# Kernel optimization log

Measured on AMD Instinct MI355X. Metric: run time of the kernel, lower is better.

The kernel has to match this reference:

```python
import jax, jax.numpy as jnp
import numpy as np

K = 7      # unfold_size
P = 3      # unfold_size // 2
EPS = 1e-5 # batchnorm eps


def _conv1x1(x, w, b=None):
    # x: (B,C,H,W), w: (O,C)
    y = jnp.einsum('bchw,oc->bohw', x, w)
    if b is not None:
        y = y + b[None, :, None, None]
    return y


def _bn(x, g, b, m, v):
    # eval-mode batchnorm over channel axis 1
    inv = jax.lax.rsqrt(v + EPS)
    return (x - m[None, :, None, None]) * (g * inv)[None, :, None, None] + b[None, :, None, None]


def setup_inputs() -> dict:
    key = jax.random.key(0)
    ks = jax.random.split(key, 18)
    B, C, MID, H, W = 8, 256, 64, 64, 64
    rn = lambda k, s, sc=1.0: jax.random.normal(k, s, dtype=jnp.float32) * sc
    ru = lambda k, s: jax.random.uniform(k, s, dtype=jnp.float32)
    return {
        'x':     rn(ks[0], (B, C, H, W)),
        'w_red': rn(ks[1], (MID, C), 0.05),
        'w_c':   rn(ks[2], (3, MID, MID, 3, 3), 0.05),
        'b_c':   rn(ks[3], (3, MID), 0.05),
        'bn_g':  ru(ks[4], (3, MID)) * 0.5 + 0.75,
        'bn_b':  rn(ks[5], (3, MID), 0.05),
        'bn_m':  rn(ks[6], (3, MID), 0.05),
        'bn_v':  ru(ks[7], (3, MID)) + 0.5,
        'w_out': rn(ks[8], (C, MID), 0.05),
        'b_out': rn(ks[9], (C,), 0.05),
        'bno_g': ru(ks[10], (C,)) * 0.5 + 0.75,
        'bno_b': rn(ks[11], (C,), 0.05),
        'bno_m': rn(ks[12], (C,), 0.05),
        'bno_v': ru(ks[13], (C,)) + 0.5,
        'w_f1':  rn(ks[14], (C, C), 0.05),
        'b_f1':  rn(ks[15], (C,), 0.05),
        'w_f2':  rn(ks[16], (C, C), 0.05),
        'b_f2':  rn(ks[17], (C,), 0.05),
    }


def reference(x, w_red, w_c, b_c, bn_g, bn_b, bn_m, bn_v,
              w_out, b_out, bno_g, bno_b, bno_m, bno_v,
              w_f1, b_f1, w_f2, b_f2):
    B, C, H, W = x.shape
    MID = w_red.shape[0]

    # channel reduction + L2 normalize over channels (F.normalize, eps=1e-12)
    q = _conv1x1(x, w_red)                                   # (B,MID,H,W)
    q = q / jnp.maximum(jnp.linalg.norm(q, axis=1, keepdims=True), 1e-12)

    # SelfCorrelationComputation: unfold KxK with padding P, multiply by center, clamp >= 0
    qp = jnp.pad(q, ((0, 0), (0, 0), (P, P), (P, P)))
    pats = jnp.stack([qp[:, :, i:i + H, j:j + W]
                      for i in range(K) for j in range(K)], axis=2)  # (B,MID,K*K,H,W)
    ss = jnp.maximum(pats * q[:, :, None], 0.0)              # (B,MID,49,H,W)

    # SelfSimilarityEncoder: conv3d with (1,ksize,ksize) kernel == batched 2D conv over (u,v)
    ss = ss.transpose(0, 3, 4, 1, 2).reshape(B * H * W, MID, K, K)  # (B*HW,MID,K,K)
    dn = ('NCHW', 'OIHW', 'NCHW')
    y = ss
    for i in range(3):  # unfold_size // 2 blocks; 7 -> 5 -> 3 -> 1
        y = jax.lax.conv_general_dilated(y, w_c[i], (1, 1), 'VALID', dimension_numbers=dn)
        y = y + b_c[i][None, :, None, None]
        y = jnp.maximum(_bn(y, bn_g[i], bn_b[i], bn_m[i], bn_v[i]), 0.0)
    y = y.mean(axis=(-1, -2)).reshape(B, H, W, MID).transpose(0, 3, 1, 2)  # (B,MID,H,W)
    feat = _bn(_conv1x1(y, w_out, b_out), bno_g, bno_b, bno_m, bno_v)      # (B,C,H,W)

    # residual + FFN (1x1 conv -> relu -> 1x1 conv)
    out = x + feat
    out = _conv1x1(jnp.maximum(_conv1x1(out, w_f1, b_f1), 0.0), w_f2, b_f2)
    return out
```

## Files before the change

### kernel.cpp

```cpp
#include <hip/hip_runtime.h>
#include <stdint.h>


typedef __attribute__((ext_vector_type(8))) __bf16 bf16x8;
typedef __attribute__((ext_vector_type(4))) float f32x4;

__device__ __forceinline__ ushort f2bf(float f) {
  __bf16 h = (__bf16)f;
  return __builtin_bit_cast(ushort, h);
}
__device__ __forceinline__ float bfu(ushort h) {
  return __builtin_bit_cast(float, ((uint32_t)h) << 16);
}
__device__ __forceinline__ f32x4 mfma16(bf16x8 a, bf16x8 b, f32x4 c) {
  return __builtin_amdgcn_mfma_f32_16x16x32_bf16(a, b, c, 0, 0, 0);
}

union BV8 { uint4 v; ushort u[8]; };

#define OFF_WRT 0u
#define OFF_WCB 65536u
#define OFF_SHC 286720u
#define OFF_WOB 287488u
#define OFF_SHO 320256u
#define OFF_WF1 321280u
#define OFF_WF2 452352u
#define OFF_QN  583424u
#define OFF_Y   4777728u

__global__ __launch_bounds__(256) void k_prep(
    const float* __restrict__ w_red, const float* __restrict__ w_c, const float* __restrict__ b_c,
    const float* __restrict__ bn_g, const float* __restrict__ bn_b, const float* __restrict__ bn_m,
    const float* __restrict__ bn_v, const float* __restrict__ w_out, const float* __restrict__ b_out,
    const float* __restrict__ bno_g, const float* __restrict__ bno_b, const float* __restrict__ bno_m,
    const float* __restrict__ bno_v, const float* __restrict__ w_f1, const float* __restrict__ w_f2,
    float* __restrict__ w_red_t, ushort* __restrict__ wc_b, float* __restrict__ shift_c,
    ushort* __restrict__ w_out_b, float* __restrict__ shift_o,
    ushort* __restrict__ w_f1_b, ushort* __restrict__ w_f2_b)
{
  int i = blockIdx.x * 256 + threadIdx.x;
  if (i < 16384) {
    int c = i >> 6, m = i & 63;
    w_red_t[i] = w_red[m * 256 + c];
    return;
  }
  i -= 16384;
  if (i < 110592) {
    int c = i & 63, o = (i >> 6) & 63, st = i >> 12;
    int tap = st % 9, s = st / 9;
    float sc = bn_g[s * 64 + o] * rsqrtf(bn_v[s * 64 + o] + 1e-5f);
    wc_b[i] = f2bf(w_c[((s * 64 + o) * 64 + c) * 9 + tap] * sc);
    return;
  }
  i -= 110592;
  if (i < 192) {
    int s = i >> 6, o = i & 63;
    float sc = bn_g[s * 64 + o] * rsqrtf(bn_v[s * 64 + o] + 1e-5f);
    shift_c[i] = (b_c[i] - bn_m[i]) * sc + bn_b[i];
    return;
  }
  i -= 192;
  if (i < 16384) {
    int o = i >> 6;
    float sc = bno_g[o] * rsqrtf(bno_v[o] + 1e-5f);
    w_out_b[i] = f2bf(w_out[i] * sc);
    return;
  }
  i -= 16384;
  if (i < 256) {
    float sc = bno_g[i] * rsqrtf(bno_v[i] + 1e-5f);
    shift_o[i] = (b_out[i] - bno_m[i]) * sc + bno_b[i];
    return;
  }
  i -= 256;
  if (i < 65536) { w_f1_b[i] = f2bf(w_f1[i]); return; }
  i -= 65536;
  if (i < 65536) { w_f2_b[i] = f2bf(w_f2[i]); return; }
}

__global__ __launch_bounds__(256) void k_qnorm(
    const float* __restrict__ x, const float* __restrict__ w_red_t, ushort* __restrict__ qn)
{
  __shared__ float xs[64 * 64];
  __shared__ float wls[64 * 64];
  __shared__ float part[64 * 16];
  __shared__ float sinv[64];

  const int tid = threadIdx.x;
  const int pix0 = blockIdx.x * 64;
  const int b = pix0 >> 12;
  const int hw0 = pix0 & 4095;
  const int pxq = tid & 15, mq = tid >> 4;
  const int lr = tid >> 2, lseg = tid & 3;

  float acc[4][4] = {};

  for (int c0 = 0; c0 < 256; c0 += 64) {
    const float4* xg = (const float4*)(x + (size_t)(b * 256 + c0 + lr) * 4096 + hw0 + lseg * 16);
    float4* xd = (float4*)(xs + lr * 64 + lseg * 16);
    const float4* wg = (const float4*)(w_red_t + (c0 + lr) * 64 + lseg * 16);
    float4* wd = (float4*)(wls + lr * 64 + lseg * 16);
#pragma unroll
    for (int j = 0; j < 4; ++j) xd[j] = xg[j];
#pragma unroll
    for (int j = 0; j < 4; ++j) wd[j] = wg[j];
    __syncthreads();
    for (int c = 0; c < 64; ++c) {
      float4 xv = *(const float4*)(xs + c * 64 + pxq * 4);
      float4 wv = *(const float4*)(wls + c * 64 + mq * 4);
      float xa[4] = {xv.x, xv.y, xv.z, xv.w};
      float wa[4] = {wv.x, wv.y, wv.z, wv.w};
#pragma unroll
      for (int mi = 0; mi < 4; ++mi)
#pragma unroll
        for (int pi = 0; pi < 4; ++pi)
          acc[mi][pi] = fmaf(wa[mi], xa[pi], acc[mi][pi]);
    }
    __syncthreads();
  }

#pragma unroll
  for (int pi = 0; pi < 4; ++pi) {
    float s = 0.f;
#pragma unroll
    for (int mi = 0; mi < 4; ++mi) s += acc[mi][pi] * acc[mi][pi];
    part[(pxq * 4 + pi) * 16 + mq] = s;
  }
  __syncthreads();
  if (tid < 64) {
    float s = 0.f;
#pragma unroll
    for (int k = 0; k < 16; ++k) s += part[tid * 16 + k];
    sinv[tid] = 1.0f / fmaxf(sqrtf(s), 1e-12f);
  }
  __syncthreads();
#pragma unroll
  for (int pi = 0; pi < 4; ++pi) {
    const int px = pxq * 4 + pi;
    const float inv = sinv[px];
    ushort4 v;
    v.x = f2bf(acc[0][pi] * inv);
    v.y = f2bf(acc[1][pi] * inv);
    v.z = f2bf(acc[2][pi] * inv);
    v.w = f2bf(acc[3][pi] * inv);
    *(ushort4*)(qn + (size_t)(pix0 + px) * 64 + mq * 4) = v;
  }
}

#define ENC_RING 7168
#define ENC_O1   14336
#define SMEM_ENC 79872

__device__ __forceinline__ void store_act(ushort* buf, int pos, int n, int q, int o0,
                                          f32x4 acc, float4 sh) {
  ushort4 v;
  v.x = f2bf(fmaxf(acc[0] + sh.x, 0.0f));
  v.y = f2bf(fmaxf(acc[1] + sh.y, 0.0f));
  v.z = f2bf(fmaxf(acc[2] + sh.z, 0.0f));
  v.w = f2bf(fmaxf(acc[3] + sh.w, 0.0f));
  const int chunk = (o0 >> 3) + (q >> 1);
  *(ushort4*)(buf + (pos * 16 + n) * 64 + ((chunk ^ (n & 7)) * 8) + (q & 1) * 4) = v;
}

__device__ __forceinline__ void build_row(
    ushort* dstslot, const ushort* __restrict__ qn,
    int b, int tr, int tc, int ir, int tid)
{
  for (int u0 = tid; u0 < 896; u0 += 256) {
    const int ch = u0 & 7, px = (u0 >> 3) & 15, dv = u0 >> 7;
    const int ph = tr + (px >> 2), pw = tc + (px & 3);
    const int nh = ph + ir - 3, nw = pw + dv - 3;
    uint4 ov4;
    if ((unsigned)nh < 64u && (unsigned)nw < 64u) {
      BV8 cv; cv.v = *(const uint4*)(qn + (size_t)((b << 12) + ph * 64 + pw) * 64 + ch * 8);
      BV8 nv; nv.v = *(const uint4*)(qn + (size_t)((b << 12) + nh * 64 + nw) * 64 + ch * 8);
      BV8 ov;
#pragma unroll
      for (int j = 0; j < 8; ++j)
        ov.u[j] = f2bf(fmaxf(bfu(nv.u[j]) * bfu(cv.u[j]), 0.0f));
      ov4 = ov.v;
    } else {
      ov4 = make_uint4(0u, 0u, 0u, 0u);
    }
    *(uint4*)(dstslot + (dv * 16 + px) * 64 + ((ch ^ (px & 7)) * 8)) = ov4;
  }
}

__global__ __launch_bounds__(256, 2) void k_encoder(
    const ushort* __restrict__ qn, const ushort* __restrict__ wc_b,
    const float* __restrict__ shift_c, ushort* __restrict__ yout)
{
  extern __shared__ char smem[];
  ushort* enc = (ushort*)smem;
  ushort* o1 = enc + ENC_O1;

  const int tid = threadIdx.x;
  const int b = blockIdx.z;
  const int tr = blockIdx.y * 4;
  const int tc = blockIdx.x * 4;

  const int lane = tid & 63, wv = tid >> 6;
  const int n = lane & 15, q = lane >> 4;
  const int o0 = wv * 16;
  const int sw = n & 7;
  const int rowoff = n * 64;
  const int c0 = ((0 + q) ^ sw) * 8;
  const int c1 = ((4 + q) ^ sw) * 8;

  bf16x8 af[18];
#pragma unroll
  for (int t = 0; t < 9; ++t) {
    af[t * 2]     = *(const bf16x8*)(wc_b + (t * 64 + o0 + n) * 64 + q * 8);
    af[t * 2 + 1] = *(const bf16x8*)(wc_b + (t * 64 + o0 + n) * 64 + 32 + q * 8);
  }

  const f32x4 zero = {0.f, 0.f, 0.f, 0.f};
  f32x4 acc[5][5];
#pragma unroll
  for (int u = 0; u < 5; ++u)
#pragma unroll
    for (int v = 0; v < 5; ++v) acc[u][v] = zero;

  build_row(enc, qn, b, tr, tc, 0, tid);
  __syncthreads();

#pragma unroll
  for (int ir = 0; ir < 7; ++ir) {
    if (ir < 6)
      build_row(enc + ((ir + 1) & 1) * ENC_RING, qn, b, tr, tc, ir + 1, tid);
    {
      const ushort* rowb = enc + (ir & 1) * ENC_RING + rowoff;
      bf16x8 rf0[7], rf1[7];
#pragma unroll
      for (int j = 0; j < 7; ++j) {
        rf0[j] = *(const bf16x8*)(rowb + j * 1024 + c0);
        rf1[j] = *(const bf16x8*)(rowb + j * 1024 + c1);
      }
#pragma unroll
      for (int u = 0; u < 5; ++u) {
        const int du = ir - u;
        if (du >= 0 && du < 3) {
#pragma unroll
          for (int dv = 0; dv < 3; ++dv)
#pragma unroll
            for (int v = 0; v < 5; ++v) {
              acc[u][v] = mfma16(af[(du * 3 + dv) * 2],     rf0[v + dv], acc[u][v]);
              acc[u][v] = mfma16(af[(du * 3 + dv) * 2 + 1], rf1[v + dv], acc[u][v]);
            }
        }
      }
    }
    if (ir < 6) __syncthreads();
  }

  {
    const float4 sh = *(const float4*)(shift_c + o0 + q * 4);
#pragma unroll
    for (int u = 0; u < 5; ++u)
#pragma unroll
      for (int v = 0; v < 5; ++v)
        store_act(o1, u * 5 + v, n, q, o0, acc[u][v], sh);
  }
  __syncthreads();

  {
#pragma unroll
    for (int t = 0; t < 9; ++t) {
      af[t * 2]     = *(const bf16x8*)(wc_b + 9 * 4096 + (t * 64 + o0 + n) * 64 + q * 8);
      af[t * 2 + 1] = *(const bf16x8*)(wc_b + 9 * 4096 + (t * 64 + o0 + n) * 64 + 32 + q * 8);
    }
    f32x4 acc2[3][3];
#pragma unroll
    for (int u = 0; u < 3; ++u)
#pragma unroll
      for (int v = 0; v < 3; ++v) acc2[u][v] = zero;

#pragma unroll
    for (int ir = 0; ir < 5; ++ir) {
      const ushort* rowb = o1 + ir * 5 * 1024 + rowoff;
      bf16x8 rf0[5], rf1[5];
#pragma unroll
      for (int j = 0; j < 5; ++j) {
        rf0[j] = *(const bf16x8*)(rowb + j * 1024 + c0);
        rf1[j] = *(const bf16x8*)(rowb + j * 1024 + c1);
      }
#pragma unroll
      for (int u = 0; u < 3; ++u) {
        const int du = ir - u;
        if (du >= 0 && du < 3) {
#pragma unroll
          for (int dv = 0; dv < 3; ++dv)
#pragma unroll
            for (int v = 0; v < 3; ++v) {
              acc2[u][v] = mfma16(af[(du * 3 + dv) * 2],     rf0[v + dv], acc2[u][v]);
              acc2[u][v] = mfma16(af[(du * 3 + dv) * 2 + 1], rf1[v + dv], acc2[u][v]);
            }
        }
      }
    }
    const float4 sh = *(const float4*)(shift_c + 64 + o0 + q * 4);
#pragma unroll
    for (int u = 0; u < 3; ++u)
#pragma unroll
      for (int v = 0; v < 3; ++v)
        store_act(enc, u * 3 + v, n, q, o0, acc2[u][v], sh);
  }
  __syncthreads();

  {
#pragma unroll
    for (int t = 0; t < 9; ++t) {
      af[t * 2]     = *(const bf16x8*)(wc_b + 18 * 4096 + (t * 64 + o0 + n) * 64 + q * 8);
      af[t * 2 + 1] = *(const bf16x8*)(wc_b + 18 * 4096 + (t * 64 + o0 + n) * 64 + 32 + q * 8);
    }
    f32x4 a0 = zero, a1 = zero;
#pragma unroll
    for (int tap = 0; tap < 9; ++tap) {
      const ushort* rA = enc + tap * 1024 + rowoff;
      a0 = mfma16(af[tap * 2],     *(const bf16x8*)(rA + c0), a0);
      a1 = mfma16(af[tap * 2 + 1], *(const bf16x8*)(rA + c1), a1);
    }
    f32x4 acc3 = a0 + a1;
    const float4 sh = *(const float4*)(shift_c + 128 + o0 + q * 4);
    ushort4 v;
    v.x = f2bf(fmaxf(acc3[0] + sh.x, 0.0f));
    v.y = f2bf(fmaxf(acc3[1] + sh.y, 0.0f));
    v.z = f2bf(fmaxf(acc3[2] + sh.z, 0.0f));
    v.w = f2bf(fmaxf(acc3[3] + sh.w, 0.0f));
    const int ph = tr + (n >> 2), pw = tc + (n & 3);
    *(ushort4*)(yout + (size_t)((b << 12) + ph * 64 + pw) * 64 + o0 + q * 4) = v;
  }
}

#define SMEM_OUT (2 * 64 * 256 * 2)

__global__ __launch_bounds__(256) void k_out(
    const ushort* __restrict__ y, const float* __restrict__ x,
    const ushort* __restrict__ w_out_b, const float* __restrict__ shift_o,
    const ushort* __restrict__ w_f1_b, const float* __restrict__ b_f1,
    const ushort* __restrict__ w_f2_b, const float* __restrict__ b_f2,
    float* __restrict__ out)
{
  extern __shared__ char smem[];
  ushort* rls = (ushort*)smem;
  ushort* hls = (ushort*)(smem + 64 * 256 * 2);

  const int tid = threadIdx.x, lane = tid & 63, wv = tid >> 6;
  const int n = lane & 15, q = lane >> 4;
  const int pix0 = blockIdx.x * 64;
  const int b = pix0 >> 12, hw0 = pix0 & 4095;
  const int sw = n & 7;
  const f32x4 zero = {0.f, 0.f, 0.f, 0.f};

  {
    bf16x8 wa[8];
#pragma unroll
    for (int mt = 0; mt < 4; ++mt) {
      const int ob = wv * 64 + mt * 16;
      wa[mt * 2]     = *(const bf16x8*)(w_out_b + (ob + n) * 64 + q * 8);
      wa[mt * 2 + 1] = *(const bf16x8*)(w_out_b + (ob + n) * 64 + 32 + q * 8);
    }
    for (int nt = 0; nt < 4; ++nt) {
      const int px0 = nt * 16;
      const bf16x8 yb0 = *(const bf16x8*)(y + (size_t)(pix0 + px0 + n) * 64 + q * 8);
      const bf16x8 yb1 = *(const bf16x8*)(y + (size_t)(pix0 + px0 + n) * 64 + 32 + q * 8);
#pragma unroll
      for (int mt = 0; mt < 4; ++mt) {
        const int ob = wv * 64 + mt * 16;
        f32x4 acc = zero;
        acc = mfma16(wa[mt * 2], yb0, acc);
        acc = mfma16(wa[mt * 2 + 1], yb1, acc);
        const float4 sh = *(const float4*)(shift_o + ob + q * 4);
        const float sha[4] = {sh.x, sh.y, sh.z, sh.w};
        ushort tmp[4];
#pragma unroll
        for (int r = 0; r < 4; ++r) {
          const int o = ob + q * 4 + r;
          const float xv = x[(size_t)(b * 256 + o) * 4096 + hw0 + px0 + n];
          tmp[r] = f2bf(xv + acc[r] + sha[r]);
        }
        ushort4 v; v.x = tmp[0]; v.y = tmp[1]; v.z = tmp[2]; v.w = tmp[3];
        const int chunk = (ob >> 3) + (q >> 1);
        *(ushort4*)(rls + (px0 + n) * 256 + ((chunk ^ sw) * 8) + (q & 1) * 4) = v;
      }
    }
  }
  __syncthreads();

  {
    bf16x8 wf[32];
#pragma unroll
    for (int mt = 0; mt < 4; ++mt)
#pragma unroll
      for (int kc = 0; kc < 8; ++kc)
        wf[mt * 8 + kc] = *(const bf16x8*)(w_f1_b + (size_t)(wv * 64 + mt * 16 + n) * 256 + kc * 32 + q * 8);
    for (int nt = 0; nt < 4; ++nt) {
      const int px0 = nt * 16;
      bf16x8 rb[8];
#pragma unroll
      for (int kc = 0; kc < 8; ++kc)
        rb[kc] = *(const bf16x8*)(rls + (px0 + n) * 256 + (((kc * 4 + q) ^ sw) * 8));
#pragma unroll
      for (int mt = 0; mt < 4; ++mt) {
        const int ob = wv * 64 + mt * 16;
        f32x4 a0 = zero, a1 = zero;
#pragma unroll
        for (int kc = 0; kc < 8; kc += 2) {
          a0 = mfma16(wf[mt * 8 + kc], rb[kc], a0);
          a1 = mfma16(wf[mt * 8 + kc + 1], rb[kc + 1], a1);
        }
        f32x4 acc = a0 + a1;
        const float4 bb = *(const float4*)(b_f1 + ob + q * 4);
        const float bba[4] = {bb.x, bb.y, bb.z, bb.w};
        ushort tmp[4];
#pragma unroll
        for (int r = 0; r < 4; ++r) tmp[r] = f2bf(fmaxf(acc[r] + bba[r], 0.0f));
        ushort4 v; v.x = tmp[0]; v.y = tmp[1]; v.z = tmp[2]; v.w = tmp[3];
        const int chunk = (ob >> 3) + (q >> 1);
        *(ushort4*)(hls + (px0 + n) * 256 + ((chunk ^ sw) * 8) + (q & 1) * 4) = v;
      }
    }
  }
  __syncthreads();

  {
    bf16x8 wf[32];
#pragma unroll
    for (int mt = 0; mt < 4; ++mt)
#pragma unroll
      for (int kc = 0; kc < 8; ++kc)
        wf[mt * 8 + kc] = *(const bf16x8*)(w_f2_b + (size_t)(wv * 64 + mt * 16 + n) * 256 + kc * 32 + q * 8);
    for (int nt = 0; nt < 4; ++nt) {
      const int px0 = nt * 16;
      bf16x8 rb[8];
#pragma unroll
      for (int kc = 0; kc < 8; ++kc)
        rb[kc] = *(const bf16x8*)(hls + (px0 + n) * 256 + (((kc * 4 + q) ^ sw) * 8));
#pragma unroll
      for (int mt = 0; mt < 4; ++mt) {
        const int ob = wv * 64 + mt * 16;
        f32x4 a0 = zero, a1 = zero;
#pragma unroll
        for (int kc = 0; kc < 8; kc += 2) {
          a0 = mfma16(wf[mt * 8 + kc], rb[kc], a0);
          a1 = mfma16(wf[mt * 8 + kc + 1], rb[kc + 1], a1);
        }
        f32x4 acc = a0 + a1;
        const float4 bb = *(const float4*)(b_f2 + ob + q * 4);
        const float bba[4] = {bb.x, bb.y, bb.z, bb.w};
#pragma unroll
        for (int r = 0; r < 4; ++r) {
          const int o = ob + q * 4 + r;
          out[(size_t)(b * 256 + o) * 4096 + hw0 + px0 + n] = acc[r] + bba[r];
        }
      }
    }
  }
}

extern "C" void kernel_launch(void* const* d_in, const int* in_sizes, int n_in,
                              void* d_out, int out_size, void* d_ws, size_t ws_size,
                              hipStream_t stream) {
  const float* x     = (const float*)d_in[0];
  const float* w_red = (const float*)d_in[1];
  const float* w_c   = (const float*)d_in[2];
  const float* b_c   = (const float*)d_in[3];
  const float* bn_g  = (const float*)d_in[4];
  const float* bn_b  = (const float*)d_in[5];
  const float* bn_m  = (const float*)d_in[6];
  const float* bn_v  = (const float*)d_in[7];
  const float* w_out = (const float*)d_in[8];
  const float* b_out = (const float*)d_in[9];
  const float* bno_g = (const float*)d_in[10];
  const float* bno_b = (const float*)d_in[11];
  const float* bno_m = (const float*)d_in[12];
  const float* bno_v = (const float*)d_in[13];
  const float* w_f1  = (const float*)d_in[14];
  const float* b_f1  = (const float*)d_in[15];
  const float* w_f2  = (const float*)d_in[16];
  const float* b_f2  = (const float*)d_in[17];

  char* ws = (char*)d_ws;
  float*  w_red_t = (float*)(ws + OFF_WRT);
  ushort* wc_b    = (ushort*)(ws + OFF_WCB);
  float*  shift_c = (float*)(ws + OFF_SHC);
  ushort* w_out_b = (ushort*)(ws + OFF_WOB);
  float*  shift_o = (float*)(ws + OFF_SHO);
  ushort* w_f1_b  = (ushort*)(ws + OFF_WF1);
  ushort* w_f2_b  = (ushort*)(ws + OFF_WF2);
  ushort* qnb     = (ushort*)(ws + OFF_QN);
  ushort* yb      = (ushort*)(ws + OFF_Y);

  k_prep<<<1074, 256, 0, stream>>>(w_red, w_c, b_c, bn_g, bn_b, bn_m, bn_v,
                                   w_out, b_out, bno_g, bno_b, bno_m, bno_v,
                                   w_f1, w_f2,
                                   w_red_t, wc_b, shift_c, w_out_b, shift_o, w_f1_b, w_f2_b);
  k_qnorm<<<512, 256, 0, stream>>>(x, w_red_t, qnb);
  k_encoder<<<dim3(16, 16, 8), 256, SMEM_ENC, stream>>>(qnb, wc_b, shift_c, yb);
  k_out<<<512, 256, SMEM_OUT, stream>>>(yb, x, w_out_b, shift_o, w_f1_b, b_f1, w_f2_b, b_f2,
                                        (float*)d_out);
}
```

Before: 276.3 us.

## Move channel-reduction GEMM in qnorm to split-bf16 MFMA

Replaces the fp32 FMA tiled GEMM for the channel reduction with bf16 MFMA instructions, using a hi/lo split of both x and w_red (three MFMAs per tile) to keep close to fp32 accuracy. Weights are pre-split in the prep kernel, and x is read directly from global memory per lane with no shared-memory staging. The norm reduction now uses wave shuffles instead of shared memory and block syncs. The risk is strided, uncoalesced-per-lane global loads of x and a small accuracy loss compared with full fp32.

```diff
diff --git a/kernel.cpp b/kernel.cpp
--- a/kernel.cpp
+++ b/kernel.cpp
@@ -17,8 +17,10 @@
 }
 
 union BV8 { uint4 v; ushort u[8]; };
-
-#define OFF_WRT 0u
+union BW8 { bf16x8 v; ushort u[8]; };
+
+#define OFF_WHI 0u
+#define OFF_WLO 32768u
 #define OFF_WCB 65536u
 #define OFF_SHC 286720u
 #define OFF_WOB 287488u
@@ -34,14 +36,17 @@
     const float* __restrict__ bn_v, const float* __restrict__ w_out, const float* __restrict__ b_out,
     const float* __restrict__ bno_g, const float* __restrict__ bno_b, const float* __restrict__ bno_m,
     const float* __restrict__ bno_v, const float* __restrict__ w_f1, const float* __restrict__ w_f2,
-    float* __restrict__ w_red_t, ushort* __restrict__ wc_b, float* __restrict__ shift_c,
+    ushort* __restrict__ w_hi, ushort* __restrict__ w_lo,
+    ushort* __restrict__ wc_b, float* __restrict__ shift_c,
     ushort* __restrict__ w_out_b, float* __restrict__ shift_o,
     ushort* __restrict__ w_f1_b, ushort* __restrict__ w_f2_b)
 {
   int i = blockIdx.x * 256 + threadIdx.x;
   if (i < 16384) {
-    int c = i >> 6, m = i & 63;
-    w_red_t[i] = w_red[m * 256 + c];
+    float w = w_red[i];
+    ushort h = f2bf(w);
+    w_hi[i] = h;
+    w_lo[i] = f2bf(w - bfu(h));
     return;
   }
   i -= 16384;
@@ -79,71 +84,60 @@
 }
 
 __global__ __launch_bounds__(256) void k_qnorm(
-    const float* __restrict__ x, const float* __restrict__ w_red_t, ushort* __restrict__ qn)
+    const float* __restrict__ x, const ushort* __restrict__ w_hi,
+    const ushort* __restrict__ w_lo, ushort* __restrict__ qn)
 {
-  __shared__ float xs[64 * 64];
-  __shared__ float wls[64 * 64];
-  __shared__ float part[64 * 16];
-  __shared__ float sinv[64];
-
-  const int tid = threadIdx.x;
+  const int tid = threadIdx.x, lane = tid & 63, wv = tid >> 6;
+  const int n = lane & 15, q = lane >> 4;
   const int pix0 = blockIdx.x * 64;
-  const int b = pix0 >> 12;
-  const int hw0 = pix0 & 4095;
-  const int pxq = tid & 15, mq = tid >> 4;
-  const int lr = tid >> 2, lseg = tid & 3;
-
-  float acc[4][4] = {};
-
-  for (int c0 = 0; c0 < 256; c0 += 64) {
-    const float4* xg = (const float4*)(x + (size_t)(b * 256 + c0 + lr) * 4096 + hw0 + lseg * 16);
-    float4* xd = (float4*)(xs + lr * 64 + lseg * 16);
-    const float4* wg = (const float4*)(w_red_t + (c0 + lr) * 64 + lseg * 16);
-    float4* wd = (float4*)(wls + lr * 64 + lseg * 16);
-#pragma unroll
-    for (int j = 0; j < 4; ++j) xd[j] = xg[j];
-#pragma unroll
-    for (int j = 0; j < 4; ++j) wd[j] = wg[j];
-    __syncthreads();
-    for (int c = 0; c < 64; ++c) {
-      float4 xv = *(const float4*)(xs + c * 64 + pxq * 4);
-      float4 wv = *(const float4*)(wls + c * 64 + mq * 4);
-      float xa[4] = {xv.x, xv.y, xv.z, xv.w};
-      float wa[4] = {wv.x, wv.y, wv.z, wv.w};
-#pragma unroll
-      for (int mi = 0; mi < 4; ++mi)
-#pragma unroll
-        for (int pi = 0; pi < 4; ++pi)
-          acc[mi][pi] = fmaf(wa[mi], xa[pi], acc[mi][pi]);
-    }
-    __syncthreads();
-  }
-
-#pragma unroll
-  for (int pi = 0; pi < 4; ++pi) {
-    float s = 0.f;
-#pragma unroll
-    for (int mi = 0; mi < 4; ++mi) s += acc[mi][pi] * acc[mi][pi];
-    part[(pxq * 4 + pi) * 16 + mq] = s;
-  }
-  __syncthreads();
-  if (tid < 64) {
-    float s = 0.f;
-#pragma unroll
-    for (int k = 0; k < 16; ++k) s += part[tid * 16 + k];
-    sinv[tid] = 1.0f / fmaxf(sqrtf(s), 1e-12f);
-  }
-  __syncthreads();
-#pragma unroll
-  for (int pi = 0; pi < 4; ++pi) {
-    const int px = pxq * 4 + pi;
-    const float inv = sinv[px];
+  const int b = pix0 >> 12, hw0 = pix0 & 4095;
+  const int pxg = hw0 + wv * 16 + n;
+  const float* xb = x + (size_t)b * 256 * 4096 + pxg;
+
+  const f32x4 zero = {0.f, 0.f, 0.f, 0.f};
+  f32x4 acc[4] = {zero, zero, zero, zero};
+
+#pragma unroll
+  for (int kk = 0; kk < 8; ++kk) {
+    const int cbase = kk * 32 + q * 8;
+    float xv[8];
+#pragma unroll
+    for (int j = 0; j < 8; ++j)
+      xv[j] = xb[(size_t)(cbase + j) * 4096];
+    BW8 xh, xl;
+#pragma unroll
+    for (int j = 0; j < 8; ++j) {
+      const ushort h = f2bf(xv[j]);
+      xh.u[j] = h;
+      xl.u[j] = f2bf(xv[j] - bfu(h));
+    }
+#pragma unroll
+    for (int mt = 0; mt < 4; ++mt) {
+      const bf16x8 wh = *(const bf16x8*)(w_hi + (mt * 16 + n) * 256 + cbase);
+      const bf16x8 wl = *(const bf16x8*)(w_lo + (mt * 16 + n) * 256 + cbase);
+      acc[mt] = mfma16(wh, xh.v, acc[mt]);
+      acc[mt] = mfma16(wh, xl.v, acc[mt]);
+      acc[mt] = mfma16(wl, xh.v, acc[mt]);
+    }
+  }
+
+  float s = 0.f;
+#pragma unroll
+  for (int mt = 0; mt < 4; ++mt)
+#pragma unroll
+    for (int r = 0; r < 4; ++r) s += acc[mt][r] * acc[mt][r];
+  s += __shfl_xor(s, 16);
+  s += __shfl_xor(s, 32);
+  const float inv = 1.0f / fmaxf(sqrtf(s), 1e-12f);
+
+#pragma unroll
+  for (int mt = 0; mt < 4; ++mt) {
     ushort4 v;
-    v.x = f2bf(acc[0][pi] * inv);
-    v.y = f2bf(acc[1][pi] * inv);
-    v.z = f2bf(acc[2][pi] * inv);
-    v.w = f2bf(acc[3][pi] * inv);
-    *(ushort4*)(qn + (size_t)(pix0 + px) * 64 + mq * 4) = v;
+    v.x = f2bf(acc[mt][0] * inv);
+    v.y = f2bf(acc[mt][1] * inv);
+    v.z = f2bf(acc[mt][2] * inv);
+    v.w = f2bf(acc[mt][3] * inv);
+    *(ushort4*)(qn + (size_t)(pix0 + wv * 16 + n) * 64 + mt * 16 + q * 4) = v;
   }
 }
 
@@ -481,7 +475,8 @@
   const float* b_f2  = (const float*)d_in[17];
 
   char* ws = (char*)d_ws;
-  float*  w_red_t = (float*)(ws + OFF_WRT);
+  ushort* w_hi    = (ushort*)(ws + OFF_WHI);
+  ushort* w_lo    = (ushort*)(ws + OFF_WLO);
   ushort* wc_b    = (ushort*)(ws + OFF_WCB);
   float*  shift_c = (float*)(ws + OFF_SHC);
   ushort* w_out_b = (ushort*)(ws + OFF_WOB);
@@ -494,8 +489,8 @@
   k_prep<<<1074, 256, 0, stream>>>(w_red, w_c, b_c, bn_g, bn_b, bn_m, bn_v,
                                    w_out, b_out, bno_g, bno_b, bno_m, bno_v,
                                    w_f1, w_f2,
-                                   w_red_t, wc_b, shift_c, w_out_b, shift_o, w_f1_b, w_f2_b);
-  k_qnorm<<<512, 256, 0, stream>>>(x, w_red_t, qnb);
+                                   w_hi, w_lo, wc_b, shift_c, w_out_b, shift_o, w_f1_b, w_f2_b);
+  k_qnorm<<<512, 256, 0, stream>>>(x, w_hi, w_lo, qnb);
   k_encoder<<<dim3(16, 16, 8), 256, SMEM_ENC, stream>>>(qnb, wc_b, shift_c, yb);
   k_out<<<512, 256, SMEM_OUT, stream>>>(yb, x, w_out_b, shift_o, w_f1_b, b_f1, w_f2_b, b_f2,
                                         (float*)d_out);
```

Measured after the change: 276.1 us. No clear change (-0.1%).
